# Kernel optimization log

Measured on AMD Instinct MI355X. Metric: run time of the kernel, lower is better.

Reference implementation:

```python
import jax, jax.numpy as jnp
import numpy as np

B, N, C_IN, C_OUT, F = 8, 2048, 256, 256, 8
EPS = 1e-4

def setup_inputs() -> dict:
    key = jax.random.key(0)
    k1, k2, k3, k4, k5 = jax.random.split(key, 5)
    node_feats = jax.random.normal(k1, (B, N, C_IN), dtype=jnp.float32)
    # sparse-ish 0/1 adjacency with self-loops already added (as module assumes)
    adj = (jax.random.uniform(k2, (B, N, N)) < 0.02).astype(jnp.float32)
    eye = jnp.eye(N, dtype=jnp.float32)[None, :, :]
    adj_matrix = jnp.maximum(adj, eye)
    filters = jax.random.normal(k3, (F, C_OUT, C_IN), dtype=jnp.float32) * (1.0 / np.sqrt(C_IN))
    proj_w = jax.random.normal(k4, (1, F), dtype=jnp.float32) * (1.0 / np.sqrt(F))
    proj_b = jax.random.normal(k5, (1,), dtype=jnp.float32) * 0.01
    return {"node_feats": node_feats, "adj_matrix": adj_matrix,
            "filters": filters, "proj_w": proj_w, "proj_b": proj_b}

def reference(node_feats, adj_matrix, filters, proj_w, proj_b):
    # Multi-head filter transform + projection over heads, fused algebraically:
    # torch: ext[b,n,k,f] = sum_i filters[f,k,i]*x[b,n,i]; x' = ext @ proj_w.T + proj_b
    x = jnp.einsum('bni,fki,f->bnk', node_feats, filters, proj_w[0]) + proj_b[0]  # [B,N,c_out]
    # adjacency-weighted aggregation + mean normalization
    num_neighbours = jnp.sum(adj_matrix, axis=-1, keepdims=True)  # [B,N,1]
    agg = jnp.einsum('bij,bjk->bik', adj_matrix, x)  # [B,N,c_out]
    return agg / (num_neighbours + EPS)
```

## Files before the change

### kernel.cpp

```cpp
#include <hip/hip_runtime.h>
#include <hip/hip_bf16.h>

#define B_DIM  8
#define N_DIM  2048
#define CIN    256
#define COUT   256
#define F_DIM  8
#define EPS    1e-4f
#define CAP    128

using short8 = __attribute__((ext_vector_type(8))) short;
using f32x4  = __attribute__((ext_vector_type(4))) float;

__device__ __forceinline__ unsigned short f2bf(float f) {
    union { float f; unsigned u; } x; x.f = f;
    unsigned r = x.u + 0x7FFFu + ((x.u >> 16) & 1u);
    return (unsigned short)(r >> 16);
}
__device__ __forceinline__ float uf(unsigned u) {
    union { unsigned u; float f; } x; x.u = u;
    return x.f;
}

__global__ __launch_bounds__(256) void wb_build(const float* __restrict__ filters,
                                                const float* __restrict__ proj_w,
                                                unsigned short* __restrict__ Wb) {
    int gid = blockIdx.x * 256 + threadIdx.x;
    float acc = 0.f;
#pragma unroll
    for (int f = 0; f < F_DIM; ++f)
        acc += proj_w[f] * filters[f * (COUT * CIN) + gid];
    Wb[gid] = f2bf(acc);
}

__global__ __launch_bounds__(256) void xp_gemm(const float* __restrict__ nf,
                                               const unsigned short* __restrict__ Wb,
                                               const float* __restrict__ proj_b,
                                               unsigned short* __restrict__ xp) {
    const int tid  = threadIdx.x;
    const int lane = tid & 63;
    const int wv   = tid >> 6;
    const int m0   = blockIdx.x * 64;
    const int lrow = lane & 15;
    const int kgrp = lane >> 4;
    const float bias = proj_b[0];

    f32x4 acc[4][4];
#pragma unroll
    for (int a = 0; a < 4; ++a)
#pragma unroll
        for (int b = 0; b < 4; ++b)
            acc[a][b] = (f32x4){0.f, 0.f, 0.f, 0.f};

#pragma unroll
    for (int ks = 0; ks < 8; ++ks) {
        const int klane = ks * 32 + kgrp * 8;
        short8 af[4], bfr[4];
#pragma unroll
        for (int fm = 0; fm < 4; ++fm) {
            const float* ap = nf + (size_t)(m0 + fm * 16 + lrow) * CIN + klane;
            float4 a0 = *(const float4*)ap;
            float4 a1 = *(const float4*)(ap + 4);
            short8 t;
            t[0] = (short)f2bf(a0.x); t[1] = (short)f2bf(a0.y);
            t[2] = (short)f2bf(a0.z); t[3] = (short)f2bf(a0.w);
            t[4] = (short)f2bf(a1.x); t[5] = (short)f2bf(a1.y);
            t[6] = (short)f2bf(a1.z); t[7] = (short)f2bf(a1.w);
            af[fm] = t;
        }
#pragma unroll
        for (int fn = 0; fn < 4; ++fn) {
            const unsigned short* bp =
                Wb + (size_t)(wv * 64 + fn * 16 + lrow) * CIN + klane;
            bfr[fn] = *(const short8*)bp;
        }
#pragma unroll
        for (int fm = 0; fm < 4; ++fm)
#pragma unroll
            for (int fn = 0; fn < 4; ++fn)
                acc[fm][fn] = __builtin_amdgcn_mfma_f32_16x16x32_bf16(
                    af[fm], bfr[fn], acc[fm][fn], 0, 0, 0);
    }

#pragma unroll
    for (int fm = 0; fm < 4; ++fm)
#pragma unroll
        for (int fn = 0; fn < 4; ++fn) {
            const int gcol = wv * 64 + fn * 16 + lrow;
#pragma unroll
            for (int r = 0; r < 4; ++r) {
                const int grow = m0 + fm * 16 + kgrp * 4 + r;
                xp[(size_t)grow * COUT + gcol] = f2bf(acc[fm][fn][r] + bias);
            }
        }
}

__global__ __launch_bounds__(256) void agg_pipe(const float* __restrict__ adj,
                                                const unsigned short* __restrict__ xp,
                                                float* __restrict__ out) {
    __shared__ __align__(16) unsigned short s_idx[4][2][CAP];

    const int tid   = threadIdx.x;
    const int lane  = tid & 63;
    const int wid   = tid >> 6;
    const int bid   = blockIdx.x;
    const int b     = bid & 7;
    const int rbase = (bid >> 3) * 32 + wid * 8;
    const int h     = lane >> 5;
    const unsigned hsh = h * 16;

    const float* arow = adj + ((size_t)b * N_DIM + rbase) * N_DIM;
    const unsigned short* xb = xp + (size_t)b * (N_DIM * COUT) + (lane & 31) * 8;

    float4 v[8];

#define ISSUE(r)                                                     \
    {                                                                \
        const float* rp = arow + (size_t)(r) * N_DIM;                \
        _Pragma("unroll")                                            \
        for (int q = 0; q < 8; ++q)                                  \
            v[q] = *(const float4*)(rp + q * 256 + lane * 4);        \
    }

    auto compact = [&](int par) -> int {
        unsigned nz = 0u;
#pragma unroll
        for (int q = 0; q < 8; ++q) {
            nz |= (v[q].x != 0.f ? 1u : 0u) << (4 * q + 0);
            nz |= (v[q].y != 0.f ? 1u : 0u) << (4 * q + 1);
            nz |= (v[q].z != 0.f ? 1u : 0u) << (4 * q + 2);
            nz |= (v[q].w != 0.f ? 1u : 0u) << (4 * q + 3);
        }
        const int c = __popc(nz);
        int pre = c;
#pragma unroll
        for (int off = 1; off < 64; off <<= 1) {
            int n = __shfl_up(pre, off, 64);
            if (lane >= off) pre += n;
        }
        const int total = __shfl(pre, 63, 64);
        int p = pre - c;
        unsigned m = nz;
        unsigned short* ib = &s_idx[wid][par][0];
        while (m) {
            int e = __builtin_ctz(m);
            m &= m - 1;
            if (p < CAP)
                ib[p] = (unsigned short)(((e >> 2) << 8) + (lane << 2) + (e & 3));
            ++p;
        }
        return total;
    };

    ISSUE(0);
    int cnt_cur = compact(0);

    for (int r = 0; r < 8; ++r) {
        if (r < 7) ISSUE(r + 1);

        const int mcnt = cnt_cur < CAP ? cnt_cur : CAP;
        const unsigned short* ib = &s_idx[wid][r & 1][0];
        float a0=0.f,a1=0.f,a2=0.f,a3=0.f,a4=0.f,a5=0.f,a6=0.f,a7=0.f;

        for (int t = 0; t < mcnt; t += 16) {
            uint4 iv0 = *(const uint4*)(ib + t);
            uint4 iv1 = *(const uint4*)(ib + t + 8);
            unsigned w[8] = {iv0.x, iv0.y, iv0.z, iv0.w, iv1.x, iv1.y, iv1.z, iv1.w};
            uint4 g[8];
#pragma unroll
            for (int k = 0; k < 8; ++k) {
                int j = (int)((w[k] >> hsh) & 0xFFFFu) & (N_DIM - 1);
                g[k] = *(const uint4*)(xb + j * COUT);
            }
#pragma unroll
            for (int k = 0; k < 8; ++k) {
                const float s = (t + 2 * k + h) < mcnt ? 1.f : 0.f;
                a0 = fmaf(s, uf(g[k].x << 16),         a0);
                a1 = fmaf(s, uf(g[k].x & 0xFFFF0000u), a1);
                a2 = fmaf(s, uf(g[k].y << 16),         a2);
                a3 = fmaf(s, uf(g[k].y & 0xFFFF0000u), a3);
                a4 = fmaf(s, uf(g[k].z << 16),         a4);
                a5 = fmaf(s, uf(g[k].z & 0xFFFF0000u), a5);
                a6 = fmaf(s, uf(g[k].w << 16),         a6);
                a7 = fmaf(s, uf(g[k].w & 0xFFFF0000u), a7);
            }
        }

        a0 += __shfl_xor(a0, 32, 64); a1 += __shfl_xor(a1, 32, 64);
        a2 += __shfl_xor(a2, 32, 64); a3 += __shfl_xor(a3, 32, 64);
        a4 += __shfl_xor(a4, 32, 64); a5 += __shfl_xor(a5, 32, 64);
        a6 += __shfl_xor(a6, 32, 64); a7 += __shfl_xor(a7, 32, 64);

        const float inv = __builtin_amdgcn_rcpf((float)cnt_cur + EPS);
        if (lane < 32) {
            float* op = out + ((size_t)b * N_DIM + rbase + r) * COUT + lane * 8;
            float4 o0 = {a0 * inv, a1 * inv, a2 * inv, a3 * inv};
            float4 o1 = {a4 * inv, a5 * inv, a6 * inv, a7 * inv};
            *(float4*)op       = o0;
            *(float4*)(op + 4) = o1;
        }

        if (r < 7) cnt_cur = compact((r + 1) & 1);
    }
#undef ISSUE
}

extern "C" void kernel_launch(void* const* d_in, const int* in_sizes, int n_in,
                              void* d_out, int out_size, void* d_ws, size_t ws_size,
                              hipStream_t stream) {
    const float* nf      = (const float*)d_in[0];
    const float* adj     = (const float*)d_in[1];
    const float* filters = (const float*)d_in[2];
    const float* proj_w  = (const float*)d_in[3];
    const float* proj_b  = (const float*)d_in[4];
    float* out = (float*)d_out;

    unsigned short* Wb = (unsigned short*)d_ws;
    unsigned short* xp = (unsigned short*)((char*)d_ws + 131072);

    wb_build<<<(COUT * CIN) / 256, 256, 0, stream>>>(filters, proj_w, Wb);
    xp_gemm <<<(B_DIM * N_DIM) / 64, 256, 0, stream>>>(nf, Wb, proj_b, xp);
    agg_pipe<<<512, 256, 0, stream>>>(adj, xp, out);
}
```

Before: 61.59 us.

## Split aggregation into producer/consumer waves with shared-memory index handoff

The aggregation kernel is restructured so two waves read and compact adjacency rows into shared-memory index lists while the other two waves gather the bf16 features and accumulate, double-buffered across phases with a block barrier between them. The grid grows from 512 to 1024 blocks of 16 rows each, and rows are assigned contiguously instead of interleaved over batches. The aim is to overlap the bandwidth-heavy adjacency streaming with the latency-bound gathers. In exchange only half the waves issue adjacency loads, and each of the nine phases ends in a __syncthreads that stalls on the slowest wave.

```diff
diff --git a/kernel.cpp b/kernel.cpp
--- a/kernel.cpp
+++ b/kernel.cpp
@@ -95,114 +95,112 @@
         }
 }
 
-__global__ __launch_bounds__(256) void agg_pipe(const float* __restrict__ adj,
-                                                const unsigned short* __restrict__ xp,
-                                                float* __restrict__ out) {
-    __shared__ __align__(16) unsigned short s_idx[4][2][CAP];
-
-    const int tid   = threadIdx.x;
-    const int lane  = tid & 63;
-    const int wid   = tid >> 6;
-    const int bid   = blockIdx.x;
-    const int b     = bid & 7;
-    const int rbase = (bid >> 3) * 32 + wid * 8;
-    const int h     = lane >> 5;
+__global__ __launch_bounds__(256) void agg_pc(const float* __restrict__ adj,
+                                              const unsigned short* __restrict__ xp,
+                                              float* __restrict__ out) {
+    __shared__ __align__(16) unsigned short idx_buf[2][2][CAP];
+    __shared__ int cnt_buf[2][2];
+
+    const int tid  = threadIdx.x;
+    const int lane = tid & 63;
+    const int wid  = tid >> 6;
+    const int bid  = blockIdx.x;
+    const int r0   = bid * 16;
+    const int b    = bid >> 7;
+
+    const unsigned short* xb = xp + (size_t)b * (N_DIM * COUT) + (lane & 31) * 8;
+    const int h = lane >> 5;
     const unsigned hsh = h * 16;
 
-    const float* arow = adj + ((size_t)b * N_DIM + rbase) * N_DIM;
-    const unsigned short* xb = xp + (size_t)b * (N_DIM * COUT) + (lane & 31) * 8;
-
-    float4 v[8];
-
-#define ISSUE(r)                                                     \
-    {                                                                \
-        const float* rp = arow + (size_t)(r) * N_DIM;                \
-        _Pragma("unroll")                                            \
-        for (int q = 0; q < 8; ++q)                                  \
-            v[q] = *(const float4*)(rp + q * 256 + lane * 4);        \
+    for (int p = 0; p < 9; ++p) {
+        if (wid < 2) {
+            if (p < 8) {
+                const int rl  = 2 * p + wid;
+                const float* row = adj + ((size_t)r0 + rl) * N_DIM;
+                float4 v[8];
+#pragma unroll
+                for (int q = 0; q < 8; ++q)
+                    v[q] = *(const float4*)(row + q * 256 + lane * 4);
+
+                unsigned nz = 0u;
+#pragma unroll
+                for (int q = 0; q < 8; ++q) {
+                    nz |= (v[q].x != 0.f ? 1u : 0u) << (4 * q + 0);
+                    nz |= (v[q].y != 0.f ? 1u : 0u) << (4 * q + 1);
+                    nz |= (v[q].z != 0.f ? 1u : 0u) << (4 * q + 2);
+                    nz |= (v[q].w != 0.f ? 1u : 0u) << (4 * q + 3);
+                }
+                const int c = __popc(nz);
+                int pre = c;
+#pragma unroll
+                for (int off = 1; off < 64; off <<= 1) {
+                    int n = __shfl_up(pre, off, 64);
+                    if (lane >= off) pre += n;
+                }
+                const int total = __shfl(pre, 63, 64);
+                int pp = pre - c;
+                unsigned m = nz;
+                unsigned short* ib = &idx_buf[p & 1][wid][0];
+                while (m) {
+                    int e = __builtin_ctz(m);
+                    m &= m - 1;
+                    if (pp < CAP)
+                        ib[pp] = (unsigned short)(((e >> 2) << 8) + (lane << 2) + (e & 3));
+                    ++pp;
+                }
+                if (lane == 0) cnt_buf[p & 1][wid] = total;
+            }
+        } else {
+            if (p >= 1) {
+                const int gw    = wid - 2;
+                const int rl    = 2 * (p - 1) + gw;
+                const int ctrue = cnt_buf[(p - 1) & 1][gw];
+                const int mcnt  = ctrue < CAP ? ctrue : CAP;
+                const unsigned short* ib = &idx_buf[(p - 1) & 1][gw][0];
+
+                float a0=0.f,a1=0.f,a2=0.f,a3=0.f,a4=0.f,a5=0.f,a6=0.f,a7=0.f;
+                for (int t = 0; t < mcnt; t += 16) {
+                    uint4 iv0 = *(const uint4*)(ib + t);
+                    uint4 iv1 = *(const uint4*)(ib + t + 8);
+                    unsigned w[8] = {iv0.x, iv0.y, iv0.z, iv0.w,
+                                     iv1.x, iv1.y, iv1.z, iv1.w};
+                    uint4 g[8];
+#pragma unroll
+                    for (int k = 0; k < 8; ++k) {
+                        int j = (int)((w[k] >> hsh) & 0xFFFFu) & (N_DIM - 1);
+                        g[k] = *(const uint4*)(xb + j * COUT);
+                    }
+#pragma unroll
+                    for (int k = 0; k < 8; ++k) {
+                        const float s = (t + 2 * k + h) < mcnt ? 1.f : 0.f;
+                        a0 = fmaf(s, uf(g[k].x << 16),         a0);
+                        a1 = fmaf(s, uf(g[k].x & 0xFFFF0000u), a1);
+                        a2 = fmaf(s, uf(g[k].y << 16),         a2);
+                        a3 = fmaf(s, uf(g[k].y & 0xFFFF0000u), a3);
+                        a4 = fmaf(s, uf(g[k].z << 16),         a4);
+                        a5 = fmaf(s, uf(g[k].z & 0xFFFF0000u), a5);
+                        a6 = fmaf(s, uf(g[k].w << 16),         a6);
+                        a7 = fmaf(s, uf(g[k].w & 0xFFFF0000u), a7);
+                    }
+                }
+
+                a0 += __shfl_xor(a0, 32, 64); a1 += __shfl_xor(a1, 32, 64);
+                a2 += __shfl_xor(a2, 32, 64); a3 += __shfl_xor(a3, 32, 64);
+                a4 += __shfl_xor(a4, 32, 64); a5 += __shfl_xor(a5, 32, 64);
+                a6 += __shfl_xor(a6, 32, 64); a7 += __shfl_xor(a7, 32, 64);
+
+                const float inv = __builtin_amdgcn_rcpf((float)ctrue + EPS);
+                if (lane < 32) {
+                    float* op = out + ((size_t)r0 + rl) * COUT + lane * 8;
+                    float4 o0 = {a0 * inv, a1 * inv, a2 * inv, a3 * inv};
+                    float4 o1 = {a4 * inv, a5 * inv, a6 * inv, a7 * inv};
+                    *(float4*)op       = o0;
+                    *(float4*)(op + 4) = o1;
+                }
+            }
+        }
+        __syncthreads();
     }
-
-    auto compact = [&](int par) -> int {
-        unsigned nz = 0u;
-#pragma unroll
-        for (int q = 0; q < 8; ++q) {
-            nz |= (v[q].x != 0.f ? 1u : 0u) << (4 * q + 0);
-            nz |= (v[q].y != 0.f ? 1u : 0u) << (4 * q + 1);
-            nz |= (v[q].z != 0.f ? 1u : 0u) << (4 * q + 2);
-            nz |= (v[q].w != 0.f ? 1u : 0u) << (4 * q + 3);
-        }
-        const int c = __popc(nz);
-        int pre = c;
-#pragma unroll
-        for (int off = 1; off < 64; off <<= 1) {
-            int n = __shfl_up(pre, off, 64);
-            if (lane >= off) pre += n;
-        }
-        const int total = __shfl(pre, 63, 64);
-        int p = pre - c;
-        unsigned m = nz;
-        unsigned short* ib = &s_idx[wid][par][0];
-        while (m) {
-            int e = __builtin_ctz(m);
-            m &= m - 1;
-            if (p < CAP)
-                ib[p] = (unsigned short)(((e >> 2) << 8) + (lane << 2) + (e & 3));
-            ++p;
-        }
-        return total;
-    };
-
-    ISSUE(0);
-    int cnt_cur = compact(0);
-
-    for (int r = 0; r < 8; ++r) {
-        if (r < 7) ISSUE(r + 1);
-
-        const int mcnt = cnt_cur < CAP ? cnt_cur : CAP;
-        const unsigned short* ib = &s_idx[wid][r & 1][0];
-        float a0=0.f,a1=0.f,a2=0.f,a3=0.f,a4=0.f,a5=0.f,a6=0.f,a7=0.f;
-
-        for (int t = 0; t < mcnt; t += 16) {
-            uint4 iv0 = *(const uint4*)(ib + t);
-            uint4 iv1 = *(const uint4*)(ib + t + 8);
-            unsigned w[8] = {iv0.x, iv0.y, iv0.z, iv0.w, iv1.x, iv1.y, iv1.z, iv1.w};
-            uint4 g[8];
-#pragma unroll
-            for (int k = 0; k < 8; ++k) {
-                int j = (int)((w[k] >> hsh) & 0xFFFFu) & (N_DIM - 1);
-                g[k] = *(const uint4*)(xb + j * COUT);
-            }
-#pragma unroll
-            for (int k = 0; k < 8; ++k) {
-                const float s = (t + 2 * k + h) < mcnt ? 1.f : 0.f;
-                a0 = fmaf(s, uf(g[k].x << 16),         a0);
-                a1 = fmaf(s, uf(g[k].x & 0xFFFF0000u), a1);
-                a2 = fmaf(s, uf(g[k].y << 16),         a2);
-                a3 = fmaf(s, uf(g[k].y & 0xFFFF0000u), a3);
-                a4 = fmaf(s, uf(g[k].z << 16),         a4);
-                a5 = fmaf(s, uf(g[k].z & 0xFFFF0000u), a5);
-                a6 = fmaf(s, uf(g[k].w << 16),         a6);
-                a7 = fmaf(s, uf(g[k].w & 0xFFFF0000u), a7);
-            }
-        }
-
-        a0 += __shfl_xor(a0, 32, 64); a1 += __shfl_xor(a1, 32, 64);
-        a2 += __shfl_xor(a2, 32, 64); a3 += __shfl_xor(a3, 32, 64);
-        a4 += __shfl_xor(a4, 32, 64); a5 += __shfl_xor(a5, 32, 64);
-        a6 += __shfl_xor(a6, 32, 64); a7 += __shfl_xor(a7, 32, 64);
-
-        const float inv = __builtin_amdgcn_rcpf((float)cnt_cur + EPS);
-        if (lane < 32) {
-            float* op = out + ((size_t)b * N_DIM + rbase + r) * COUT + lane * 8;
-            float4 o0 = {a0 * inv, a1 * inv, a2 * inv, a3 * inv};
-            float4 o1 = {a4 * inv, a5 * inv, a6 * inv, a7 * inv};
-            *(float4*)op       = o0;
-            *(float4*)(op + 4) = o1;
-        }
-
-        if (r < 7) cnt_cur = compact((r + 1) & 1);
-    }
-#undef ISSUE
 }
 
 extern "C" void kernel_launch(void* const* d_in, const int* in_sizes, int n_in,
@@ -220,5 +218,5 @@
 
     wb_build<<<(COUT * CIN) / 256, 256, 0, stream>>>(filters, proj_w, Wb);
     xp_gemm <<<(B_DIM * N_DIM) / 64, 256, 0, stream>>>(nf, Wb, proj_b, xp);
-    agg_pipe<<<512, 256, 0, stream>>>(adj, xp, out);
-}
+    agg_pc  <<<(B_DIM * N_DIM) / 16, 256, 0, stream>>>(adj, xp, out);
+}
```

Result: slower. 89.13 us (+44.7%).
